# Performance work log

Hardware: AMD Instinct MI355X
Metric: run time of the kernel (lower is better)

The kernel has to match this reference:

```python
import jax, jax.numpy as jnp
import numpy as np
from jax import lax

EPS = 1e-15
MAX_TANH = 1.0 - 1e-5


def _artanh(x):
    x = jnp.clip(x, -MAX_TANH, MAX_TANH)
    return jnp.arctanh(x)


def mobius_add(x, y):
    # Poincare ball, c=1 (geoopt create_ball default)
    x2 = jnp.sum(x * x, axis=-1, keepdims=True)
    y2 = jnp.sum(y * y, axis=-1, keepdims=True)
    xy = jnp.sum(x * y, axis=-1, keepdims=True)
    num = (1.0 + 2.0 * xy + y2) * x + (1.0 - x2) * y
    den = 1.0 + 2.0 * xy + x2 * y2
    return num / jnp.maximum(den, EPS)


def mobius_matvec(x, W):
    # geoopt: mobius_matvec(weight.T, x) == hyperbolic version of x @ W
    x_norm = jnp.maximum(jnp.linalg.norm(x, axis=-1, keepdims=True), EPS)
    mx = x @ W
    mx_norm = jnp.maximum(jnp.linalg.norm(mx, axis=-1, keepdims=True), EPS)
    res = jnp.tanh(mx_norm / x_norm * _artanh(x_norm)) * (mx / mx_norm)
    return jnp.where(mx_norm <= 1e-10, jnp.zeros_like(res), res)


def logmap0(y):
    yn = jnp.maximum(jnp.linalg.norm(y, axis=-1, keepdims=True), EPS)
    return _artanh(yn) * y / yn


def expmap0(u):
    un = jnp.maximum(jnp.linalg.norm(u, axis=-1, keepdims=True), EPS)
    return jnp.tanh(un) * u / un


def setup_inputs() -> dict:
    key = jax.random.key(0)
    k1, k2, k3, k4 = jax.random.split(key, 4)
    N, IN, OUT, DEG = 20000, 512, 256, 16
    feat = jax.random.normal(k1, (N, IN), dtype=jnp.float32) * 0.02    # points near origin of ball
    weight = jax.random.normal(k2, (IN, OUT), dtype=jnp.float32) * (1.0 / np.sqrt(IN))
    bias = jax.random.normal(k3, (OUT,), dtype=jnp.float32) * 0.01
    src = jax.random.randint(k4, (N, DEG), 0, N, dtype=jnp.int32)      # in-neighbors per node
    return {"feat": feat, "weight": weight, "bias": bias, "src": src}


def reference(feat, weight, bias, src):
    N, deg = src.shape
    norm = jnp.asarray(deg, feat.dtype) ** -0.5  # in_degrees == deg for all nodes
    h = feat * norm
    # in_feats > out_feats branch: transform before aggregation
    h = mobius_matvec(h, weight)                 # [N, OUT]
    msgs = h[src]                                # gather mailbox [N, deg, OUT]
    # sequential left-fold with mobius_add over neighbors (non-associative)
    carry = msgs[:, 0]
    rest = jnp.moveaxis(msgs[:, 1:], 1, 0)       # [deg-1, N, OUT]

    def step(c, m):
        return mobius_add(c, m), None

    rst, _ = lax.scan(step, carry, rest)
    rst = rst * norm
    rst = mobius_add(rst, bias)
    rst = expmap0(jax.nn.relu(logmap0(rst)))     # hyperbolic relu
    return rst
```

## Files before the change

kernel.cpp:

```cpp
#include <hip/hip_runtime.h>
#include <hip/hip_fp16.h>
#include <math.h>

#define EPSF 1e-15f
#define MAX_TANH_F (1.0f - 1e-5f)
#define KDIM 512
#define NOUT 256
#define BM 32
#define BK 64

typedef __attribute__((ext_vector_type(8))) __bf16 bf16x8;
typedef __attribute__((ext_vector_type(4))) float f32x4;

#define BAR_TILE() asm volatile("s_waitcnt vmcnt(8) lgkmcnt(0)\n\ts_barrier" ::: "memory")

__device__ __forceinline__ void gload_lds16(const float* g, float* l) {
    __builtin_amdgcn_global_load_lds(
        (const __attribute__((address_space(1))) void*)g,
        (__attribute__((address_space(3))) void*)l, 16, 0, 0);
}

__device__ __forceinline__ float artanh_clip(float x) {
    x = fminf(fmaxf(x, -MAX_TANH_F), MAX_TANH_F);
    return atanhf(x);
}

__device__ __forceinline__ void unpack2h(unsigned int u, float& a, float& b) {
    __half2 hh = __builtin_bit_cast(__half2, u);
    a = __low2float(hh);
    b = __high2float(hh);
}

__device__ __forceinline__ bf16x8 cvt8(const float4& a, const float4& b) {
    bf16x8 r;
    r[0] = (__bf16)a.x; r[1] = (__bf16)a.y; r[2] = (__bf16)a.z; r[3] = (__bf16)a.w;
    r[4] = (__bf16)b.x; r[5] = (__bf16)b.y; r[6] = (__bf16)b.z; r[7] = (__bf16)b.w;
    return r;
}
__device__ __forceinline__ float sq8(const float4& a, const float4& b) {
    return a.x*a.x + a.y*a.y + a.z*a.z + a.w*a.w
         + b.x*b.x + b.y*b.y + b.z*b.z + b.w*b.w;
}

__global__ __launch_bounds__(64) void prep_w_kernel(
    const float* __restrict__ W, unsigned int* __restrict__ Wp)
{
    const int b = blockIdx.x;
    const int l = threadIdx.x;
    const int k0 = (b >> 4) * 32 + (l >> 4) * 8;
    const int col = (b & 15) * 16 + (l & 15);
    bf16x8 v;
    #pragma unroll
    for (int j = 0; j < 8; ++j) v[j] = (__bf16)W[(size_t)(k0 + j) * NOUT + col];
    *(uint4*)(Wp + ((size_t)b * 64 + l) * 4) = __builtin_bit_cast(uint4, v);
}

__global__ __launch_bounds__(256) void gemm_mobius_kernel(
    const float* __restrict__ feat, const uint4* __restrict__ Wp,
    __half* __restrict__ h, float* __restrict__ hnorm2,
    float scale, int N)
{
    __shared__ float lds_a[2][BM * BK];
    __shared__ float sred[4][BM];
    __shared__ float sfac[BM];
    __shared__ float sxn2[BM];

    const int tid  = threadIdx.x;
    const int wave = tid >> 6;
    const int lane = tid & 63;
    const int rr   = lane & 15;
    const int g    = lane >> 4;
    const int base = blockIdx.x * BM;

    const int row0  = wave * 4 + (lane >> 4);
    const int row1  = 16 + row0;
    const int s16x  = (lane & 15) ^ (row0 & 15);
    const int gr0 = base + row0 < N ? base + row0 : N - 1;
    const int gr1 = base + row1 < N ? base + row1 : N - 1;
    const float* gs0 = feat + (size_t)gr0 * KDIM + s16x * 4;
    const float* gs1 = feat + (size_t)gr1 * KDIM + s16x * 4;

    f32x4 acc[2][4];
    #pragma unroll
    for (int hh = 0; hh < 2; ++hh)
        #pragma unroll
        for (int t = 0; t < 4; ++t) acc[hh][t] = (f32x4){0.f, 0.f, 0.f, 0.f};

    const uint4* wp = Wp + (size_t)wave * 4 * 64 + lane;

    gload_lds16(gs0, &lds_a[0][(wave * 4) * BK]);
    gload_lds16(gs1, &lds_a[0][(16 + wave * 4) * BK]);
    __builtin_amdgcn_sched_barrier(0);

    uint4 B[2][4];
    #pragma unroll
    for (int p = 0; p < 2; ++p)
        #pragma unroll
        for (int t = 0; t < 4; ++t)
            B[p][t] = wp[((size_t)p * 16 + t) * 64];

    BAR_TILE();

    float xs0 = 0.f, xs1 = 0.f;

    #pragma unroll
    for (int kk = 0; kk < 8; ++kk) {
        if (kk < 7) {
            float* db = &lds_a[(kk + 1) & 1][0];
            gload_lds16(gs0 + (kk + 1) * BK, db + (wave * 4) * BK);
            gload_lds16(gs1 + (kk + 1) * BK, db + (16 + wave * 4) * BK);
            __builtin_amdgcn_sched_barrier(0);
        }

        const float* buf = lds_a[kk & 1];
        #pragma unroll
        for (int ss = 0; ss < 2; ++ss) {
            const int s = kk * 2 + ss;
            const int ls0 = ((ss * 8 + g * 2)     ^ rr) * 4;
            const int ls1 = ((ss * 8 + g * 2 + 1) ^ rr) * 4;
            float4 a00 = *(const float4*)(buf + rr * BK + ls0);
            float4 a01 = *(const float4*)(buf + rr * BK + ls1);
            float4 a10 = *(const float4*)(buf + (16 + rr) * BK + ls0);
            float4 a11 = *(const float4*)(buf + (16 + rr) * BK + ls1);
            xs0 += sq8(a00, a01);
            xs1 += sq8(a10, a11);
            bf16x8 ah0 = cvt8(a00, a01);
            bf16x8 ah1 = cvt8(a10, a11);
            uint4 b0 = B[s & 1][0], b1 = B[s & 1][1], b2 = B[s & 1][2], b3 = B[s & 1][3];
            if (s + 2 < 16) {
                #pragma unroll
                for (int t = 0; t < 4; ++t)
                    B[s & 1][t] = wp[((size_t)(s + 2) * 16 + t) * 64];
            }
            acc[0][0] = __builtin_amdgcn_mfma_f32_16x16x32_bf16(ah0, __builtin_bit_cast(bf16x8, b0), acc[0][0], 0, 0, 0);
            acc[1][0] = __builtin_amdgcn_mfma_f32_16x16x32_bf16(ah1, __builtin_bit_cast(bf16x8, b0), acc[1][0], 0, 0, 0);
            acc[0][1] = __builtin_amdgcn_mfma_f32_16x16x32_bf16(ah0, __builtin_bit_cast(bf16x8, b1), acc[0][1], 0, 0, 0);
            acc[1][1] = __builtin_amdgcn_mfma_f32_16x16x32_bf16(ah1, __builtin_bit_cast(bf16x8, b1), acc[1][1], 0, 0, 0);
            acc[0][2] = __builtin_amdgcn_mfma_f32_16x16x32_bf16(ah0, __builtin_bit_cast(bf16x8, b2), acc[0][2], 0, 0, 0);
            acc[1][2] = __builtin_amdgcn_mfma_f32_16x16x32_bf16(ah1, __builtin_bit_cast(bf16x8, b2), acc[1][2], 0, 0, 0);
            acc[0][3] = __builtin_amdgcn_mfma_f32_16x16x32_bf16(ah0, __builtin_bit_cast(bf16x8, b3), acc[0][3], 0, 0, 0);
            acc[1][3] = __builtin_amdgcn_mfma_f32_16x16x32_bf16(ah1, __builtin_bit_cast(bf16x8, b3), acc[1][3], 0, 0, 0);
        }
        if (kk < 7) BAR_TILE();
    }

    xs0 += __shfl_xor(xs0, 16); xs0 += __shfl_xor(xs0, 32);
    xs1 += __shfl_xor(xs1, 16); xs1 += __shfl_xor(xs1, 32);
    if (wave == 0 && lane < 16) { sxn2[lane] = xs0; sxn2[16 + lane] = xs1; }

    #pragma unroll
    for (int hh = 0; hh < 2; ++hh) {
        #pragma unroll
        for (int r = 0; r < 4; ++r) {
            float p = 0.f;
            #pragma unroll
            for (int t = 0; t < 4; ++t) p += acc[hh][t][r] * acc[hh][t][r];
            p += __shfl_xor(p, 1);
            p += __shfl_xor(p, 2);
            p += __shfl_xor(p, 4);
            p += __shfl_xor(p, 8);
            if (rr == 0) sred[wave][hh * 16 + g * 4 + r] = p;
        }
    }
    __syncthreads();

    if (tid < BM) {
        const int r = tid;
        const float mx2 = sred[0][r] + sred[1][r] + sred[2][r] + sred[3][r];
        const float mxn = fmaxf(scale * sqrtf(mx2), EPSF);
        const float xn  = fmaxf(scale * sqrtf(sxn2[r]), EPSF);
        float ttv = tanhf(mxn / xn * artanh_clip(xn));
        float fc  = ttv * scale / mxn;
        if (mxn <= 1e-10f) { fc = 0.f; ttv = 0.f; }
        sfac[r] = fc;
        if (base + r < N) hnorm2[base + r] = ttv * ttv;
    }
    __syncthreads();

    #pragma unroll
    for (int hh = 0; hh < 2; ++hh) {
        #pragma unroll
        for (int r = 0; r < 4; ++r) {
            const int row_r = base + hh * 16 + g * 4 + r;
            if (row_r < N) {
                const float fc = sfac[hh * 16 + g * 4 + r];
                __half* hr = h + (size_t)row_r * NOUT + wave * 64 + rr;
                #pragma unroll
                for (int t = 0; t < 4; ++t) hr[t * 16] = __float2half(acc[hh][t][r] * fc);
            }
        }
    }
}

__global__ __launch_bounds__(256) void aggregate_kernel(
    const __half* __restrict__ h, const float* __restrict__ hnorm2,
    const int* __restrict__ src, const float* __restrict__ bias,
    float* __restrict__ out, float scale, int N)
{
    const int wave = threadIdx.x >> 6;
    const int lane = threadIdx.x & 63;
    const int n0 = (blockIdx.x * 4 + wave) * 4;
    if (n0 >= N) return;
    const int g = lane >> 4;
    const int q = lane & 15;
    const int myrow = n0 + g;
    const bool rowok = myrow < N;

    size_t smax = (size_t)N * 16 - 1;
    size_t soff = (size_t)n0 * 16 + lane;
    int sidx = src[soff <= smax ? soff : smax];
    float y2v = hnorm2[sidx];

    int idx[16];
    float y2[16];
    #pragma unroll
    for (int j = 0; j < 16; ++j) {
        idx[j] = __shfl(sidx, (lane & 48) + j);
        y2[j]  = __shfl(y2v, (lane & 48) + j);
    }

    uint4 ya[16], yb[16];
    #pragma unroll
    for (int j = 0; j < 16; ++j) {
        const uint4* hp = (const uint4*)(h + (size_t)idx[j] * NOUT);
        ya[j] = hp[q * 2];
        yb[j] = hp[q * 2 + 1];
    }
    #pragma unroll
    for (int j = 0; j < 16; ++j) {
        asm volatile("" : "+v"(ya[j].x), "+v"(ya[j].y), "+v"(ya[j].z), "+v"(ya[j].w),
                          "+v"(yb[j].x), "+v"(yb[j].y), "+v"(yb[j].z), "+v"(yb[j].w));
    }

    float c[16];
    unpack2h(ya[0].x, c[0], c[1]);   unpack2h(ya[0].y, c[2], c[3]);
    unpack2h(ya[0].z, c[4], c[5]);   unpack2h(ya[0].w, c[6], c[7]);
    unpack2h(yb[0].x, c[8], c[9]);   unpack2h(yb[0].y, c[10], c[11]);
    unpack2h(yb[0].z, c[12], c[13]); unpack2h(yb[0].w, c[14], c[15]);
    float c2 = y2[0];

    #pragma unroll
    for (int j = 1; j < 16; ++j) {
        float yv[16];
        unpack2h(ya[j].x, yv[0], yv[1]);   unpack2h(ya[j].y, yv[2], yv[3]);
        unpack2h(ya[j].z, yv[4], yv[5]);   unpack2h(ya[j].w, yv[6], yv[7]);
        unpack2h(yb[j].x, yv[8], yv[9]);   unpack2h(yb[j].y, yv[10], yv[11]);
        unpack2h(yb[j].z, yv[12], yv[13]); unpack2h(yb[j].w, yv[14], yv[15]);

        float xp = 0.f;
        #pragma unroll
        for (int i = 0; i < 16; ++i) xp = fmaf(c[i], yv[i], xp);
        xp += __shfl_xor(xp, 1);
        xp += __shfl_xor(xp, 2);
        xp += __shfl_xor(xp, 4);
        xp += __shfl_xor(xp, 8);
        const float xy = xp;

        const float A = 1.f + 2.f * xy + y2[j];
        const float B = 1.f - c2;
        const float den = fmaxf(1.f + 2.f * xy + c2 * y2[j], EPSF);
        const float inv = __builtin_amdgcn_rcpf(den);
        #pragma unroll
        for (int i = 0; i < 16; ++i) c[i] = (fmaf(A, c[i], B * yv[i])) * inv;
        c2 = fmaxf((A * A * c2 + 2.f * A * B * xy + B * B * y2[j]) * (inv * inv), 0.f);
    }

    #pragma unroll
    for (int i = 0; i < 16; ++i) c[i] *= scale;
    c2 *= scale * scale;

    float bv[16];
    {
        const float4* bp = (const float4*)(bias + q * 16);
        float4 b0 = bp[0], b1 = bp[1], b2 = bp[2], b3 = bp[3];
        bv[0]=b0.x; bv[1]=b0.y; bv[2]=b0.z; bv[3]=b0.w;
        bv[4]=b1.x; bv[5]=b1.y; bv[6]=b1.z; bv[7]=b1.w;
        bv[8]=b2.x; bv[9]=b2.y; bv[10]=b2.z; bv[11]=b2.w;
        bv[12]=b3.x; bv[13]=b3.y; bv[14]=b3.z; bv[15]=b3.w;
    }
    float bp_ = 0.f, xp_ = 0.f;
    #pragma unroll
    for (int i = 0; i < 16; ++i) { bp_ = fmaf(bv[i], bv[i], bp_); xp_ = fmaf(c[i], bv[i], xp_); }
    bp_ += __shfl_xor(bp_, 1); xp_ += __shfl_xor(xp_, 1);
    bp_ += __shfl_xor(bp_, 2); xp_ += __shfl_xor(xp_, 2);
    bp_ += __shfl_xor(bp_, 4); xp_ += __shfl_xor(xp_, 4);
    bp_ += __shfl_xor(bp_, 8); xp_ += __shfl_xor(xp_, 8);
    const float bb = bp_, xy = xp_;

    const float A = 1.f + 2.f * xy + bb;
    const float B = 1.f - c2;
    const float den = fmaxf(1.f + 2.f * xy + c2 * bb, EPSF);
    const float inv = 1.f / den;
    float r4[16];
    #pragma unroll
    for (int i = 0; i < 16; ++i) r4[i] = fmaf(A, c[i], B * bv[i]) * inv;
    const float rn2 = fmaxf((A * A * c2 + 2.f * A * B * xy + B * B * bb) * (inv * inv), 0.f);

    const float rn = fmaxf(sqrtf(rn2), EPSF);
    const float lf = artanh_clip(rn) / rn;
    float u[16];
    float up = 0.f;
    #pragma unroll
    for (int i = 0; i < 16; ++i) { u[i] = fmaxf(r4[i] * lf, 0.f); up = fmaf(u[i], u[i], up); }
    up += __shfl_xor(up, 1);
    up += __shfl_xor(up, 2);
    up += __shfl_xor(up, 4);
    up += __shfl_xor(up, 8);
    const float un = fmaxf(sqrtf(up), EPSF);
    const float ef = tanhf(un) / un;

    if (rowok) {
        float* op = out + (size_t)myrow * NOUT + q * 16;
        float4 o;
        o.x = u[0]*ef;  o.y = u[1]*ef;  o.z = u[2]*ef;  o.w = u[3]*ef;  ((float4*)op)[0] = o;
        o.x = u[4]*ef;  o.y = u[5]*ef;  o.z = u[6]*ef;  o.w = u[7]*ef;  ((float4*)op)[1] = o;
        o.x = u[8]*ef;  o.y = u[9]*ef;  o.z = u[10]*ef; o.w = u[11]*ef; ((float4*)op)[2] = o;
        o.x = u[12]*ef; o.y = u[13]*ef; o.z = u[14]*ef; o.w = u[15]*ef; ((float4*)op)[3] = o;
    }
}

extern "C" void kernel_launch(void* const* d_in, const int* in_sizes, int n_in,
                              void* d_out, int out_size, void* d_ws, size_t ws_size,
                              hipStream_t stream) {
    const float* feat   = (const float*)d_in[0];
    const float* weight = (const float*)d_in[1];
    const float* bias   = (const float*)d_in[2];
    const int*   src    = (const int*)d_in[3];

    const int OUT = in_sizes[2];
    const int IN  = in_sizes[1] / OUT;
    const int N   = in_sizes[0] / IN;
    const int DEG = in_sizes[3] / N;
    (void)IN; (void)DEG; (void)out_size; (void)ws_size; (void)n_in;

    const float scale = 1.0f / sqrtf((float)DEG);

    char* ws = (char*)d_ws;
    __half* h     = (__half*)ws;
    float* hnorm2 = (float*)(ws + (size_t)N * NOUT * 2);
    unsigned int* Wp = (unsigned int*)(ws + (size_t)N * NOUT * 2 + (size_t)N * 4);

    float* out = (float*)d_out;

    const int nbm = (N + BM - 1) / BM;

    hipLaunchKernelGGL(prep_w_kernel, dim3(256), dim3(64), 0, stream,
                       weight, Wp);
    hipLaunchKernelGGL(gemm_mobius_kernel, dim3(nbm), dim3(256), 0, stream,
                       feat, (const uint4*)Wp, h, hnorm2, scale, N);
    hipLaunchKernelGGL(aggregate_kernel, dim3((N + 15) / 16), dim3(256), 0, stream,
                       h, hnorm2, src, bias, out, scale, N);
}
```

Baseline: 54.22 us.

## Use 32 lanes per node with rolling prefetch in aggregate kernel

The aggregate kernel now assigns two nodes per wave, 32 lanes each holding 8 features, instead of four nodes with 16 lanes and 16 features each. The up-front load of all 16 neighbor rows into registers is replaced by a 4-deep rolling prefetch buffer. The aim is to cut register pressure so more waves fit per CU, and to issue narrower coalesced 16-byte loads. In exchange each reduction needs an extra shuffle step, the grid doubles, and fewer loads are in flight per wave.

```diff
diff --git a/kernel.cpp b/kernel.cpp
--- a/kernel.cpp
+++ b/kernel.cpp
@@ -199,15 +199,15 @@
 {
     const int wave = threadIdx.x >> 6;
     const int lane = threadIdx.x & 63;
-    const int n0 = (blockIdx.x * 4 + wave) * 4;
+    const int n0 = (blockIdx.x * 4 + wave) * 2;
     if (n0 >= N) return;
-    const int g = lane >> 4;
-    const int q = lane & 15;
-    const int myrow = n0 + g;
+    const int g1 = lane >> 5;
+    const int q5 = lane & 31;
+    const int myrow = n0 + g1;
     const bool rowok = myrow < N;
 
     size_t smax = (size_t)N * 16 - 1;
-    size_t soff = (size_t)n0 * 16 + lane;
+    size_t soff = (size_t)n0 * 16 + q5;
     int sidx = src[soff <= smax ? soff : smax];
     float y2v = hnorm2[sidx];
 
@@ -215,45 +215,40 @@
     float y2[16];
     #pragma unroll
     for (int j = 0; j < 16; ++j) {
-        idx[j] = __shfl(sidx, (lane & 48) + j);
-        y2[j]  = __shfl(y2v, (lane & 48) + j);
-    }
-
-    uint4 ya[16], yb[16];
-    #pragma unroll
-    for (int j = 0; j < 16; ++j) {
-        const uint4* hp = (const uint4*)(h + (size_t)idx[j] * NOUT);
-        ya[j] = hp[q * 2];
-        yb[j] = hp[q * 2 + 1];
-    }
-    #pragma unroll
-    for (int j = 0; j < 16; ++j) {
-        asm volatile("" : "+v"(ya[j].x), "+v"(ya[j].y), "+v"(ya[j].z), "+v"(ya[j].w),
-                          "+v"(yb[j].x), "+v"(yb[j].y), "+v"(yb[j].z), "+v"(yb[j].w));
-    }
-
-    float c[16];
-    unpack2h(ya[0].x, c[0], c[1]);   unpack2h(ya[0].y, c[2], c[3]);
-    unpack2h(ya[0].z, c[4], c[5]);   unpack2h(ya[0].w, c[6], c[7]);
-    unpack2h(yb[0].x, c[8], c[9]);   unpack2h(yb[0].y, c[10], c[11]);
-    unpack2h(yb[0].z, c[12], c[13]); unpack2h(yb[0].w, c[14], c[15]);
+        idx[j] = __shfl(sidx, g1 * 16 + j);
+        y2[j]  = __shfl(y2v, g1 * 16 + j);
+    }
+
+    uint4 cur;
+    cur = ((const uint4*)(h + (size_t)idx[0] * NOUT))[q5];
+    uint4 pa[4];
+    #pragma unroll
+    for (int p = 0; p < 4; ++p)
+        pa[p] = ((const uint4*)(h + (size_t)idx[p + 1] * NOUT))[q5];
+
+    float c[8];
+    unpack2h(cur.x, c[0], c[1]); unpack2h(cur.y, c[2], c[3]);
+    unpack2h(cur.z, c[4], c[5]); unpack2h(cur.w, c[6], c[7]);
     float c2 = y2[0];
 
     #pragma unroll
     for (int j = 1; j < 16; ++j) {
-        float yv[16];
-        unpack2h(ya[j].x, yv[0], yv[1]);   unpack2h(ya[j].y, yv[2], yv[3]);
-        unpack2h(ya[j].z, yv[4], yv[5]);   unpack2h(ya[j].w, yv[6], yv[7]);
-        unpack2h(yb[j].x, yv[8], yv[9]);   unpack2h(yb[j].y, yv[10], yv[11]);
-        unpack2h(yb[j].z, yv[12], yv[13]); unpack2h(yb[j].w, yv[14], yv[15]);
+        const int slot = (j - 1) & 3;
+        uint4 p0 = pa[slot];
+        if (j + 4 < 16)
+            pa[slot] = ((const uint4*)(h + (size_t)idx[j + 4] * NOUT))[q5];
+        float yv[8];
+        unpack2h(p0.x, yv[0], yv[1]); unpack2h(p0.y, yv[2], yv[3]);
+        unpack2h(p0.z, yv[4], yv[5]); unpack2h(p0.w, yv[6], yv[7]);
 
         float xp = 0.f;
         #pragma unroll
-        for (int i = 0; i < 16; ++i) xp = fmaf(c[i], yv[i], xp);
+        for (int i = 0; i < 8; ++i) xp = fmaf(c[i], yv[i], xp);
         xp += __shfl_xor(xp, 1);
         xp += __shfl_xor(xp, 2);
         xp += __shfl_xor(xp, 4);
         xp += __shfl_xor(xp, 8);
+        xp += __shfl_xor(xp, 16);
         const float xy = xp;
 
         const float A = 1.f + 2.f * xy + y2[j];
@@ -261,61 +256,59 @@
         const float den = fmaxf(1.f + 2.f * xy + c2 * y2[j], EPSF);
         const float inv = __builtin_amdgcn_rcpf(den);
         #pragma unroll
-        for (int i = 0; i < 16; ++i) c[i] = (fmaf(A, c[i], B * yv[i])) * inv;
+        for (int i = 0; i < 8; ++i) c[i] = (fmaf(A, c[i], B * yv[i])) * inv;
         c2 = fmaxf((A * A * c2 + 2.f * A * B * xy + B * B * y2[j]) * (inv * inv), 0.f);
     }
 
     #pragma unroll
-    for (int i = 0; i < 16; ++i) c[i] *= scale;
+    for (int i = 0; i < 8; ++i) c[i] *= scale;
     c2 *= scale * scale;
 
-    float bv[16];
+    float bv[8];
     {
-        const float4* bp = (const float4*)(bias + q * 16);
-        float4 b0 = bp[0], b1 = bp[1], b2 = bp[2], b3 = bp[3];
+        const float4* bp = (const float4*)(bias + q5 * 8);
+        float4 b0 = bp[0], b1 = bp[1];
         bv[0]=b0.x; bv[1]=b0.y; bv[2]=b0.z; bv[3]=b0.w;
         bv[4]=b1.x; bv[5]=b1.y; bv[6]=b1.z; bv[7]=b1.w;
-        bv[8]=b2.x; bv[9]=b2.y; bv[10]=b2.z; bv[11]=b2.w;
-        bv[12]=b3.x; bv[13]=b3.y; bv[14]=b3.z; bv[15]=b3.w;
     }
     float bp_ = 0.f, xp_ = 0.f;
     #pragma unroll
-    for (int i = 0; i < 16; ++i) { bp_ = fmaf(bv[i], bv[i], bp_); xp_ = fmaf(c[i], bv[i], xp_); }
-    bp_ += __shfl_xor(bp_, 1); xp_ += __shfl_xor(xp_, 1);
-    bp_ += __shfl_xor(bp_, 2); xp_ += __shfl_xor(xp_, 2);
-    bp_ += __shfl_xor(bp_, 4); xp_ += __shfl_xor(xp_, 4);
-    bp_ += __shfl_xor(bp_, 8); xp_ += __shfl_xor(xp_, 8);
+    for (int i = 0; i < 8; ++i) { bp_ = fmaf(bv[i], bv[i], bp_); xp_ = fmaf(c[i], bv[i], xp_); }
+    bp_ += __shfl_xor(bp_, 1);  xp_ += __shfl_xor(xp_, 1);
+    bp_ += __shfl_xor(bp_, 2);  xp_ += __shfl_xor(xp_, 2);
+    bp_ += __shfl_xor(bp_, 4);  xp_ += __shfl_xor(xp_, 4);
+    bp_ += __shfl_xor(bp_, 8);  xp_ += __shfl_xor(xp_, 8);
+    bp_ += __shfl_xor(bp_, 16); xp_ += __shfl_xor(xp_, 16);
     const float bb = bp_, xy = xp_;
 
     const float A = 1.f + 2.f * xy + bb;
     const float B = 1.f - c2;
     const float den = fmaxf(1.f + 2.f * xy + c2 * bb, EPSF);
     const float inv = 1.f / den;
-    float r4[16];
-    #pragma unroll
-    for (int i = 0; i < 16; ++i) r4[i] = fmaf(A, c[i], B * bv[i]) * inv;
+    float r4[8];
+    #pragma unroll
+    for (int i = 0; i < 8; ++i) r4[i] = fmaf(A, c[i], B * bv[i]) * inv;
     const float rn2 = fmaxf((A * A * c2 + 2.f * A * B * xy + B * B * bb) * (inv * inv), 0.f);
 
     const float rn = fmaxf(sqrtf(rn2), EPSF);
     const float lf = artanh_clip(rn) / rn;
-    float u[16];
+    float u[8];
     float up = 0.f;
     #pragma unroll
-    for (int i = 0; i < 16; ++i) { u[i] = fmaxf(r4[i] * lf, 0.f); up = fmaf(u[i], u[i], up); }
+    for (int i = 0; i < 8; ++i) { u[i] = fmaxf(r4[i] * lf, 0.f); up = fmaf(u[i], u[i], up); }
     up += __shfl_xor(up, 1);
     up += __shfl_xor(up, 2);
     up += __shfl_xor(up, 4);
     up += __shfl_xor(up, 8);
+    up += __shfl_xor(up, 16);
     const float un = fmaxf(sqrtf(up), EPSF);
     const float ef = tanhf(un) / un;
 
     if (rowok) {
-        float* op = out + (size_t)myrow * NOUT + q * 16;
+        float* op = out + (size_t)myrow * NOUT + q5 * 8;
         float4 o;
-        o.x = u[0]*ef;  o.y = u[1]*ef;  o.z = u[2]*ef;  o.w = u[3]*ef;  ((float4*)op)[0] = o;
-        o.x = u[4]*ef;  o.y = u[5]*ef;  o.z = u[6]*ef;  o.w = u[7]*ef;  ((float4*)op)[1] = o;
-        o.x = u[8]*ef;  o.y = u[9]*ef;  o.z = u[10]*ef; o.w = u[11]*ef; ((float4*)op)[2] = o;
-        o.x = u[12]*ef; o.y = u[13]*ef; o.z = u[14]*ef; o.w = u[15]*ef; ((float4*)op)[3] = o;
+        o.x = u[0]*ef; o.y = u[1]*ef; o.z = u[2]*ef; o.w = u[3]*ef; ((float4*)op)[0] = o;
+        o.x = u[4]*ef; o.y = u[5]*ef; o.z = u[6]*ef; o.w = u[7]*ef; ((float4*)op)[1] = o;
     }
 }
 
@@ -348,6 +341,6 @@
                        weight, Wp);
     hipLaunchKernelGGL(gemm_mobius_kernel, dim3(nbm), dim3(256), 0, stream,
                        feat, (const uint4*)Wp, h, hnorm2, scale, N);
-    hipLaunchKernelGGL(aggregate_kernel, dim3((N + 15) / 16), dim3(256), 0, stream,
+    hipLaunchKernelGGL(aggregate_kernel, dim3((N + 7) / 8), dim3(256), 0, stream,
                        h, hnorm2, src, bias, out, scale, N);
 }
```

New measurement: 53.83 us. About the same (-0.7%).
